# Optimization experiments

Hardware: AMD Instinct MI355X
Metric: run time of the kernel (lower is better)

Reference implementation:

```python
import jax, jax.numpy as jnp
import numpy as np

IN_F, OUT_F = 256, 256
GRID, ORDER = 5, 3
K = GRID + ORDER + 1  # 9 knots
EPS_MINMAX = 1e-7     # K.epsilon()
EPS_BN = 1e-3         # keras BatchNormalization default epsilon


def setup_inputs() -> dict:
    key = jax.random.key(0)
    ks = jax.random.split(key, 4)
    x = jax.random.normal(ks[0], (32, 32, 32, IN_F), dtype=jnp.float32)
    he = lambda k, shape, fan_in: jax.random.normal(k, shape, jnp.float32) * np.sqrt(2.0 / fan_in)
    base_weight = he(ks[1], (IN_F, OUT_F), IN_F)
    spline_weight = he(ks[2], (OUT_F, IN_F, K), IN_F * K)
    spline_scaler = jnp.ones((OUT_F, IN_F), jnp.float32)
    return {
        'x': x,
        'base_weight': base_weight,
        'spline_weight': spline_weight,
        'spline_scaler': spline_scaler,
        'bn_base_gamma': jnp.ones((OUT_F,), jnp.float32),
        'bn_base_beta': jnp.zeros((OUT_F,), jnp.float32),
        'bn_base_mean': jnp.zeros((OUT_F,), jnp.float32),
        'bn_base_var': jnp.ones((OUT_F,), jnp.float32),
        'bn_spline_gamma': jnp.ones((OUT_F,), jnp.float32),
        'bn_spline_beta': jnp.zeros((OUT_F,), jnp.float32),
        'bn_spline_mean': jnp.zeros((OUT_F,), jnp.float32),
        'bn_spline_var': jnp.ones((OUT_F,), jnp.float32),
    }


def _bn(z, gamma, beta, mean, var):
    # Keras BatchNormalization, inference mode (training=False)
    return gamma * (z - mean) * jax.lax.rsqrt(var + EPS_BN) + beta


def reference(x, base_weight, spline_weight, spline_scaler,
              bn_base_gamma, bn_base_beta, bn_base_mean, bn_base_var,
              bn_spline_gamma, bn_spline_beta, bn_spline_mean, bn_spline_var):
    B, H, W, _ = x.shape
    xf = x.reshape(-1, IN_F)  # [N, in]

    # base path: GEMM -> BN -> SiLU
    base = xf @ base_weight
    base = jax.nn.silu(_bn(base, bn_base_gamma, bn_base_beta, bn_base_mean, bn_base_var))

    # min-max normalize per feature over the flattened batch
    x_min = jnp.min(xf, axis=0, keepdims=True)
    x_max = jnp.max(xf, axis=0, keepdims=True)
    xn = (xf - x_min) / (x_max - x_min + EPS_MINMAX)

    # triangle basis: relu(1 - |x - knot|), knots = linspace(-1, 1, K)
    knots = jnp.linspace(-1.0, 1.0, K, dtype=jnp.float32)
    basis = jnp.maximum(0.0, 1.0 - jnp.abs(xn[:, :, None] - knots[None, None, :]))  # [N, in, K]

    # scaled spline weight, flattened GEMM
    w = (spline_weight * spline_scaler[:, :, None]).reshape(OUT_F, IN_F * K)  # [out, in*K]
    spline = basis.reshape(-1, IN_F * K) @ w.T  # [N, out]
    spline = _bn(spline, bn_spline_gamma, bn_spline_beta, bn_spline_mean, bn_spline_var)

    out = base + spline
    return out.reshape(B, H, W, OUT_F)
```

## Files before the change

### kernel.cpp

```cpp
#include <hip/hip_runtime.h>
#include <stdint.h>
#include <stddef.h>

typedef _Float16 h2 __attribute__((ext_vector_type(2)));
typedef _Float16 h8 __attribute__((ext_vector_type(8)));
typedef float f4 __attribute__((ext_vector_type(4)));

union Hfrag { h2 p[4]; h8 v; };

#define WS_PMIN   0
#define WS_PMAX   524288
#define WS_BT     0
#define WS_SMALL  1310720
#define WS_MINV   (WS_SMALL + 0)
#define WS_SCALEV (WS_SMALL + 1024)
#define WS_BSC    (WS_SMALL + 2048)
#define WS_BSH    (WS_SMALL + 3072)
#define WS_SSC    (WS_SMALL + 4096)
#define WS_SSH    (WS_SMALL + 5120)

__global__ __launch_bounds__(256) void kan_minmax(const float* __restrict__ x,
                                                  float* __restrict__ pmin,
                                                  float* __restrict__ pmax) {
  __shared__ f4 smn[4][64], smx[4][64];
  const int b = blockIdx.x, t = threadIdx.x;
  const int fq = t & 63, rg = t >> 6;
  const float* p = x + (size_t)b * 64 * 256 + (size_t)rg * 16 * 256 + fq * 4;
  f4 mn = (f4)(3.402823466e38f), mx = (f4)(-3.402823466e38f);
#pragma unroll
  for (int j = 0; j < 16; ++j) {
    f4 v = *(const f4*)(p + (size_t)j * 256);
    mn = __builtin_elementwise_min(mn, v);
    mx = __builtin_elementwise_max(mx, v);
  }
  smn[rg][fq] = mn; smx[rg][fq] = mx;
  __syncthreads();
  if (rg == 0) {
#pragma unroll
    for (int g = 1; g < 4; ++g) {
      mn = __builtin_elementwise_min(mn, smn[g][fq]);
      mx = __builtin_elementwise_max(mx, smx[g][fq]);
    }
    *(f4*)(pmin + (size_t)b * 256 + fq * 4) = mn;
    *(f4*)(pmax + (size_t)b * 256 + fq * 4) = mx;
  }
}

__global__ __launch_bounds__(256) void kan_finalize(
    const float* __restrict__ pmin, const float* __restrict__ pmax,
    const float* __restrict__ g1, const float* __restrict__ b1,
    const float* __restrict__ m1, const float* __restrict__ v1,
    const float* __restrict__ g2, const float* __restrict__ b2,
    const float* __restrict__ m2, const float* __restrict__ v2,
    float* __restrict__ minv, float* __restrict__ scalev,
    float* __restrict__ bscv, float* __restrict__ bshv,
    float* __restrict__ sscv, float* __restrict__ sshv) {
  __shared__ float smn[4][64], smx[4][64];
  const int t = threadIdx.x;
  const int ol = t & 63, pg = t >> 6;
  const int o = blockIdx.x * 64 + ol;
  float mn = 3.402823466e38f, mx = -3.402823466e38f;
  for (int p = pg * 128; p < pg * 128 + 128; ++p) {
    mn = fminf(mn, pmin[(size_t)p * 256 + o]);
    mx = fmaxf(mx, pmax[(size_t)p * 256 + o]);
  }
  smn[pg][ol] = mn; smx[pg][ol] = mx;
  __syncthreads();
  if (pg == 0) {
#pragma unroll
    for (int g = 1; g < 4; ++g) {
      mn = fminf(mn, smn[g][ol]);
      mx = fmaxf(mx, smx[g][ol]);
    }
    minv[o] = mn;
    scalev[o] = 1.0f / (mx - mn + 1e-7f);
    const float bs = g1[o] / sqrtf(v1[o] + 1e-3f);
    bscv[o] = bs;
    bshv[o] = b1[o] - m1[o] * bs;
    const float ss = g2[o] / sqrtf(v2[o] + 1e-3f);
    sscv[o] = ss;
    sshv[o] = b2[o] - m2[o] * ss;
  }
}

__global__ __launch_bounds__(256) void kan_buildw(
    const float* __restrict__ spline_w, const float* __restrict__ spline_s,
    const float* __restrict__ base_w, _Float16* __restrict__ Bt) {
  const int gid = blockIdx.x * 256 + threadIdx.x;
  const int f = gid * 4;
  const int ks = f >> 13;
  const int rem = f & 8191;
  const int half = rem >> 12;
  const int rem2 = rem & 4095;
  const int o = rem2 >> 5;
  const int kk = rem2 & 31;
  const int og = half * 128 + o;
  float v[4];
  if (ks < 72) {
    const int k = ks >> 3;
    const int i0 = ((ks & 7) << 5) + kk;
#pragma unroll
    for (int j = 0; j < 4; ++j) {
      const int i = i0 + j;
      v[j] = spline_w[(size_t)(og * 256 + i) * 9 + k] * spline_s[og * 256 + i];
    }
  } else {
    const int i0 = (ks - 72) * 32 + kk;
#pragma unroll
    for (int j = 0; j < 4; ++j) {
      const int i = i0 + j;
      v[j] = base_w[(size_t)i * 256 + og];
    }
  }
  union { _Float16 h[4]; uint2 u; } pk;
#pragma unroll
  for (int j = 0; j < 4; ++j) pk.h[j] = (_Float16)v[j];
  *(uint2*)(Bt + f) = pk.u;
}

__global__ __launch_bounds__(256, 2) void kan_gemm(
    const float* __restrict__ x, const _Float16* __restrict__ Bt,
    const float* __restrict__ minv, const float* __restrict__ scalev,
    const float* __restrict__ bscv, const float* __restrict__ bshv,
    const float* __restrict__ sscv, const float* __restrict__ sshv,
    float* __restrict__ out) {
  const int tid = threadIdx.x;
  const int lane = tid & 63;
  const int wv = tid >> 6;
  const int wm = wv >> 1, wn = wv & 1;
  const int lr = lane & 15, lg = lane >> 4;
  const int mt = blockIdx.x & 255, nt = blockIdx.x >> 8;

  const int rowA = mt * 128 + wm * 64 + lr;
  const int colB = wn * 64 + lr;

  f4 accS[4][4], accB[4][4];
#pragma unroll
  for (int m = 0; m < 4; ++m)
#pragma unroll
    for (int n = 0; n < 4; ++n) { accS[m][n] = (f4)0.0f; accB[m][n] = (f4)0.0f; }

  const char* btbase = (const char*)Bt + (size_t)nt * 8192 + (size_t)colB * 64 + (size_t)lg * 16;

  f4 xa[4], xb[4], mn0, mn1, sc0, sc1;

  {
    const int ib = lg * 8;
#pragma unroll
    for (int m = 0; m < 4; ++m) {
      const float* px = x + (size_t)(rowA + m * 16) * 256 + ib;
      xa[m] = *(const f4*)px; xb[m] = *(const f4*)(px + 4);
    }
    mn0 = *(const f4*)(minv + ib);  mn1 = *(const f4*)(minv + ib + 4);
    sc0 = *(const f4*)(scalev + ib); sc1 = *(const f4*)(scalev + ib + 4);
  }

#pragma unroll 1
  for (int ic = 0; ic < 8; ++ic) {
    Hfrag xn[4];
#pragma unroll
    for (int m = 0; m < 4; ++m) {
      f4 na = (xa[m] - mn0) * sc0;
      f4 nb = (xb[m] - mn1) * sc1;
      xn[m].p[0][0] = (_Float16)na.x; xn[m].p[0][1] = (_Float16)na.y;
      xn[m].p[1][0] = (_Float16)na.z; xn[m].p[1][1] = (_Float16)na.w;
      xn[m].p[2][0] = (_Float16)nb.x; xn[m].p[2][1] = (_Float16)nb.y;
      xn[m].p[3][0] = (_Float16)nb.z; xn[m].p[3][1] = (_Float16)nb.w;
    }
#pragma unroll
    for (int it = 0; it < 9; ++it) {
      const int cks = (it < 8) ? ((it + 1) * 8 + ic) : (72 + ic);
      const char* bp = btbase + (size_t)cks * 16384;
      Hfrag bf[4];
#pragma unroll
      for (int n = 0; n < 4; ++n)
        bf[n].v = *(const h8*)(bp + n * 1024);
      if (it < 8) {
        const float t = -1.0f + 0.25f * (float)(it + 1);
        const _Float16 c1 = (_Float16)(1.0f + t);
        const _Float16 c2 = (_Float16)(1.0f - t);
        h2 hc1; hc1[0] = c1; hc1[1] = c1;
        h2 hc2; hc2[0] = c2; hc2[1] = c2;
        h2 hz;  hz[0] = (_Float16)0.0f; hz[1] = (_Float16)0.0f;
        Hfrag af[4];
#pragma unroll
        for (int m = 0; m < 4; ++m) {
#pragma unroll
          for (int q = 0; q < 4; ++q) {
            h2 xv = xn[m].p[q];
            h2 u = hc1 - xv;
            h2 w = hc2 + xv;
            af[m].p[q] = __builtin_elementwise_max(__builtin_elementwise_min(u, w), hz);
          }
        }
#pragma unroll
        for (int m = 0; m < 4; ++m)
#pragma unroll
          for (int n = 0; n < 4; ++n)
            accS[m][n] = __builtin_amdgcn_mfma_f32_16x16x32_f16(af[m].v, bf[n].v, accS[m][n], 0, 0, 0);
      } else {
        Hfrag af[4];
#pragma unroll
        for (int m = 0; m < 4; ++m) {
          af[m].p[0][0] = (_Float16)xa[m].x; af[m].p[0][1] = (_Float16)xa[m].y;
          af[m].p[1][0] = (_Float16)xa[m].z; af[m].p[1][1] = (_Float16)xa[m].w;
          af[m].p[2][0] = (_Float16)xb[m].x; af[m].p[2][1] = (_Float16)xb[m].y;
          af[m].p[3][0] = (_Float16)xb[m].z; af[m].p[3][1] = (_Float16)xb[m].w;
        }
#pragma unroll
        for (int m = 0; m < 4; ++m)
#pragma unroll
          for (int n = 0; n < 4; ++n)
            accB[m][n] = __builtin_amdgcn_mfma_f32_16x16x32_f16(af[m].v, bf[n].v, accB[m][n], 0, 0, 0);
        if (ic < 7) {
          const int ib = (ic + 1) * 32 + lg * 8;
#pragma unroll
          for (int m = 0; m < 4; ++m) {
            const float* px = x + (size_t)(rowA + m * 16) * 256 + ib;
            xa[m] = *(const f4*)px; xb[m] = *(const f4*)(px + 4);
          }
          mn0 = *(const f4*)(minv + ib);  mn1 = *(const f4*)(minv + ib + 4);
          sc0 = *(const f4*)(scalev + ib); sc1 = *(const f4*)(scalev + ib + 4);
        }
      }
    }
  }

#pragma unroll
  for (int n = 0; n < 4; ++n) {
    const int col = nt * 128 + colB + n * 16;
    const float vbs = bscv[col], vbh = bshv[col];
    const float vss = sscv[col], vsh = sshv[col];
#pragma unroll
    for (int m = 0; m < 4; ++m) {
      const int row0 = mt * 128 + wm * 64 + m * 16 + lg * 4;
#pragma unroll
      for (int r = 0; r < 4; ++r) {
        const float zb = accB[m][n][r] * vbs + vbh;
        const float si = zb / (1.0f + __expf(-zb));
        const float val = si + accS[m][n][r] * vss + vsh;
        out[(size_t)(row0 + r) * 256 + col] = val;
      }
    }
  }
}

extern "C" void kernel_launch(void* const* d_in, const int* in_sizes, int n_in,
                              void* d_out, int out_size, void* d_ws, size_t ws_size,
                              hipStream_t stream) {
  const float* x        = (const float*)d_in[0];
  const float* base_w   = (const float*)d_in[1];
  const float* spline_w = (const float*)d_in[2];
  const float* spline_s = (const float*)d_in[3];
  const float* g1 = (const float*)d_in[4];
  const float* b1 = (const float*)d_in[5];
  const float* m1 = (const float*)d_in[6];
  const float* v1 = (const float*)d_in[7];
  const float* g2 = (const float*)d_in[8];
  const float* b2 = (const float*)d_in[9];
  const float* m2 = (const float*)d_in[10];
  const float* v2 = (const float*)d_in[11];
  float* out = (float*)d_out;
  char* ws = (char*)d_ws;

  float* pmin   = (float*)(ws + WS_PMIN);
  float* pmax   = (float*)(ws + WS_PMAX);
  _Float16* Bt  = (_Float16*)(ws + WS_BT);
  float* minv   = (float*)(ws + WS_MINV);
  float* scalev = (float*)(ws + WS_SCALEV);
  float* bscv   = (float*)(ws + WS_BSC);
  float* bshv   = (float*)(ws + WS_BSH);
  float* sscv   = (float*)(ws + WS_SSC);
  float* sshv   = (float*)(ws + WS_SSH);

  kan_minmax<<<512, 256, 0, stream>>>(x, pmin, pmax);
  kan_finalize<<<4, 256, 0, stream>>>(pmin, pmax, g1, b1, m1, v1, g2, b2, m2, v2,
                                      minv, scalev, bscv, bshv, sscv, sshv);
  kan_buildw<<<640, 256, 0, stream>>>(spline_w, spline_s, base_w, Bt);
  kan_gemm<<<512, 256, 0, stream>>>(x, Bt, minv, scalev, bscv, bshv, sscv, sshv, out);
}
```

Baseline: 167.2 us.

## Re-express triangle basis as ReLU hinge basis to shrink spline GEMM K

Since xn is in [0,1], only knots 1..8 matter, and the hat functions are rewritten as a constant, a linear term and three ReLU hinges relu(x - b_j) on raw x. The spline K dimension drops from 8 to 4 blocks per input, and the per-knot min/max/sub work becomes one sub plus a max. Weight build folds the combined coefficients, scale and constant term (C0) into a 4-slice Bt and the BN shift, and B-fragment loads are software-prefetched one step ahead. In exchange the hinge thresholds are computed in fp16 in absolute x units, which may change precision, and the build kernel now does a shared-memory reduction.

```diff
diff --git a/kernel.cpp b/kernel.cpp
--- a/kernel.cpp
+++ b/kernel.cpp
@@ -11,13 +11,14 @@
 #define WS_PMIN   0
 #define WS_PMAX   524288
 #define WS_BT     0
-#define WS_SMALL  1310720
-#define WS_MINV   (WS_SMALL + 0)
-#define WS_SCALEV (WS_SMALL + 1024)
-#define WS_BSC    (WS_SMALL + 2048)
-#define WS_BSH    (WS_SMALL + 3072)
-#define WS_SSC    (WS_SMALL + 4096)
-#define WS_SSH    (WS_SMALL + 5120)
+#define WS_SMALL  1048576
+#define WS_SCALEV (WS_SMALL + 0)
+#define WS_BKN    (WS_SMALL + 1024)
+#define WS_C0     (WS_SMALL + 3072)
+#define WS_BSC    (WS_SMALL + 4096)
+#define WS_BSH    (WS_SMALL + 5120)
+#define WS_SSC    (WS_SMALL + 6144)
+#define WS_SSH    (WS_SMALL + 7168)
 
 __global__ __launch_bounds__(256) void kan_minmax(const float* __restrict__ x,
                                                   float* __restrict__ pmin,
@@ -52,7 +53,7 @@
     const float* __restrict__ m1, const float* __restrict__ v1,
     const float* __restrict__ g2, const float* __restrict__ b2,
     const float* __restrict__ m2, const float* __restrict__ v2,
-    float* __restrict__ minv, float* __restrict__ scalev,
+    float* __restrict__ scalev, _Float16* __restrict__ bkn,
     float* __restrict__ bscv, float* __restrict__ bshv,
     float* __restrict__ sscv, float* __restrict__ sshv) {
   __shared__ float smn[4][64], smx[4][64];
@@ -72,8 +73,12 @@
       mn = fminf(mn, smn[g][ol]);
       mx = fmaxf(mx, smx[g][ol]);
     }
-    minv[o] = mn;
-    scalev[o] = 1.0f / (mx - mn + 1e-7f);
+    const float rng = mx - mn + 1e-7f;
+    scalev[o] = 1.0f / rng;
+    const float step = 0.25f * rng;
+#pragma unroll
+    for (int j = 0; j < 4; ++j)
+      bkn[j * 256 + o] = (_Float16)(mn + step * (float)j);
     const float bs = g1[o] / sqrtf(v1[o] + 1e-3f);
     bscv[o] = bs;
     bshv[o] = b1[o] - m1[o] * bs;
@@ -85,42 +90,43 @@
 
 __global__ __launch_bounds__(256) void kan_buildw(
     const float* __restrict__ spline_w, const float* __restrict__ spline_s,
-    const float* __restrict__ base_w, _Float16* __restrict__ Bt) {
-  const int gid = blockIdx.x * 256 + threadIdx.x;
-  const int f = gid * 4;
-  const int ks = f >> 13;
-  const int rem = f & 8191;
-  const int half = rem >> 12;
-  const int rem2 = rem & 4095;
-  const int o = rem2 >> 5;
-  const int kk = rem2 & 31;
-  const int og = half * 128 + o;
-  float v[4];
-  if (ks < 72) {
-    const int k = ks >> 3;
-    const int i0 = ((ks & 7) << 5) + kk;
-#pragma unroll
-    for (int j = 0; j < 4; ++j) {
-      const int i = i0 + j;
-      v[j] = spline_w[(size_t)(og * 256 + i) * 9 + k] * spline_s[og * 256 + i];
-    }
-  } else {
-    const int i0 = (ks - 72) * 32 + kk;
-#pragma unroll
-    for (int j = 0; j < 4; ++j) {
-      const int i = i0 + j;
-      v[j] = base_w[(size_t)i * 256 + og];
-    }
-  }
-  union { _Float16 h[4]; uint2 u; } pk;
-#pragma unroll
-  for (int j = 0; j < 4; ++j) pk.h[j] = (_Float16)v[j];
-  *(uint2*)(Bt + f) = pk.u;
+    const float* __restrict__ base_w, const float* __restrict__ scalev,
+    _Float16* __restrict__ Bt, float* __restrict__ C0) {
+  const int og = blockIdx.x;
+  const int i  = threadIdx.x;
+  const float* wp = spline_w + (size_t)(og * 256 + i) * 9;
+  const float w1 = wp[1], w2 = wp[2], w3 = wp[3], w4 = wp[4];
+  const float w5 = wp[5], w6 = wp[6], w7 = wp[7], w8 = wp[8];
+  const float s  = spline_s[og * 256 + i];
+  const float sc = scalev[i];
+  const float wp0 = 0.25f*w1 + 0.5f*w2 + 0.75f*w3 + w4 + 0.75f*w5 + 0.5f*w6 + 0.25f*w7;
+  float wj[4];
+  wj[0] = (w5 + w6 + w7 + w8) - (w1 + w2 + w3 + w4);
+  wj[1] = w1 - 2.0f * w5;
+  wj[2] = w2 - 2.0f * w6;
+  wj[3] = w3 - 2.0f * w7;
+  const float ssc = s * sc;
+  const int half = og >> 7, o = og & 127, ic = i >> 5, kk = i & 31;
+#pragma unroll
+  for (int j = 0; j < 4; ++j) {
+    const int ks = j * 8 + ic;
+    Bt[((size_t)(ks * 2 + half) * 128 + o) * 32 + kk] = (_Float16)(wj[j] * ssc);
+  }
+  Bt[((size_t)((32 + ic) * 2 + half) * 128 + o) * 32 + kk] =
+      (_Float16)base_w[(size_t)i * 256 + og];
+  __shared__ float red[256];
+  red[i] = wp0 * s;
+  __syncthreads();
+  for (int st = 128; st > 0; st >>= 1) {
+    if (i < st) red[i] += red[i + st];
+    __syncthreads();
+  }
+  if (i == 0) C0[og] = red[0];
 }
 
 __global__ __launch_bounds__(256, 2) void kan_gemm(
     const float* __restrict__ x, const _Float16* __restrict__ Bt,
-    const float* __restrict__ minv, const float* __restrict__ scalev,
+    const _Float16* __restrict__ bkn, const float* __restrict__ C0,
     const float* __restrict__ bscv, const float* __restrict__ bshv,
     const float* __restrict__ sscv, const float* __restrict__ sshv,
     float* __restrict__ out) {
@@ -142,8 +148,9 @@
 
   const char* btbase = (const char*)Bt + (size_t)nt * 8192 + (size_t)colB * 64 + (size_t)lg * 16;
 
-  f4 xa[4], xb[4], mn0, mn1, sc0, sc1;
-
+  h2 hz; hz[0] = (_Float16)0.0f; hz[1] = (_Float16)0.0f;
+
+  f4 xa[4], xb[4];
   {
     const int ib = lg * 8;
 #pragma unroll
@@ -151,77 +158,70 @@
       const float* px = x + (size_t)(rowA + m * 16) * 256 + ib;
       xa[m] = *(const f4*)px; xb[m] = *(const f4*)(px + 4);
     }
-    mn0 = *(const f4*)(minv + ib);  mn1 = *(const f4*)(minv + ib + 4);
-    sc0 = *(const f4*)(scalev + ib); sc1 = *(const f4*)(scalev + ib + 4);
   }
 
 #pragma unroll 1
   for (int ic = 0; ic < 8; ++ic) {
-    Hfrag xn[4];
+    Hfrag bb[4];
+#pragma unroll
+    for (int j = 0; j < 4; ++j)
+      bb[j].v = *(const h8*)(bkn + j * 256 + ic * 32 + lg * 8);
+
+    Hfrag xh[4];
 #pragma unroll
     for (int m = 0; m < 4; ++m) {
-      f4 na = (xa[m] - mn0) * sc0;
-      f4 nb = (xb[m] - mn1) * sc1;
-      xn[m].p[0][0] = (_Float16)na.x; xn[m].p[0][1] = (_Float16)na.y;
-      xn[m].p[1][0] = (_Float16)na.z; xn[m].p[1][1] = (_Float16)na.w;
-      xn[m].p[2][0] = (_Float16)nb.x; xn[m].p[2][1] = (_Float16)nb.y;
-      xn[m].p[3][0] = (_Float16)nb.z; xn[m].p[3][1] = (_Float16)nb.w;
-    }
-#pragma unroll
-    for (int it = 0; it < 9; ++it) {
-      const int cks = (it < 8) ? ((it + 1) * 8 + ic) : (72 + ic);
-      const char* bp = btbase + (size_t)cks * 16384;
-      Hfrag bf[4];
-#pragma unroll
-      for (int n = 0; n < 4; ++n)
-        bf[n].v = *(const h8*)(bp + n * 1024);
-      if (it < 8) {
-        const float t = -1.0f + 0.25f * (float)(it + 1);
-        const _Float16 c1 = (_Float16)(1.0f + t);
-        const _Float16 c2 = (_Float16)(1.0f - t);
-        h2 hc1; hc1[0] = c1; hc1[1] = c1;
-        h2 hc2; hc2[0] = c2; hc2[1] = c2;
-        h2 hz;  hz[0] = (_Float16)0.0f; hz[1] = (_Float16)0.0f;
+      xh[m].p[0][0] = (_Float16)xa[m].x; xh[m].p[0][1] = (_Float16)xa[m].y;
+      xh[m].p[1][0] = (_Float16)xa[m].z; xh[m].p[1][1] = (_Float16)xa[m].w;
+      xh[m].p[2][0] = (_Float16)xb[m].x; xh[m].p[2][1] = (_Float16)xb[m].y;
+      xh[m].p[3][0] = (_Float16)xb[m].z; xh[m].p[3][1] = (_Float16)xb[m].w;
+    }
+
+    if (ic < 7) {
+      const int ib = (ic + 1) * 32 + lg * 8;
+#pragma unroll
+      for (int m = 0; m < 4; ++m) {
+        const float* px = x + (size_t)(rowA + m * 16) * 256 + ib;
+        xa[m] = *(const f4*)px; xb[m] = *(const f4*)(px + 4);
+      }
+    }
+
+    const char* bpic = btbase + (size_t)ic * 16384;
+    Hfrag bf[4];
+#pragma unroll
+    for (int n = 0; n < 4; ++n) bf[n].v = *(const h8*)(bpic + n * 1024);
+
+#pragma unroll
+    for (int it = 0; it < 5; ++it) {
+      Hfrag bnx[4];
+      if (it < 4) {
+        const char* bp = bpic + (size_t)(it + 1) * 131072;
+#pragma unroll
+        for (int n = 0; n < 4; ++n) bnx[n].v = *(const h8*)(bp + n * 1024);
+      }
+      if (it < 4) {
         Hfrag af[4];
 #pragma unroll
-        for (int m = 0; m < 4; ++m) {
+        for (int m = 0; m < 4; ++m)
 #pragma unroll
           for (int q = 0; q < 4; ++q) {
-            h2 xv = xn[m].p[q];
-            h2 u = hc1 - xv;
-            h2 w = hc2 + xv;
-            af[m].p[q] = __builtin_elementwise_max(__builtin_elementwise_min(u, w), hz);
+            h2 d = xh[m].p[q] - bb[it].p[q];
+            af[m].p[q] = __builtin_elementwise_max(d, hz);
           }
-        }
 #pragma unroll
         for (int m = 0; m < 4; ++m)
 #pragma unroll
           for (int n = 0; n < 4; ++n)
             accS[m][n] = __builtin_amdgcn_mfma_f32_16x16x32_f16(af[m].v, bf[n].v, accS[m][n], 0, 0, 0);
       } else {
-        Hfrag af[4];
-#pragma unroll
-        for (int m = 0; m < 4; ++m) {
-          af[m].p[0][0] = (_Float16)xa[m].x; af[m].p[0][1] = (_Float16)xa[m].y;
-          af[m].p[1][0] = (_Float16)xa[m].z; af[m].p[1][1] = (_Float16)xa[m].w;
-          af[m].p[2][0] = (_Float16)xb[m].x; af[m].p[2][1] = (_Float16)xb[m].y;
-          af[m].p[3][0] = (_Float16)xb[m].z; af[m].p[3][1] = (_Float16)xb[m].w;
-        }
 #pragma unroll
         for (int m = 0; m < 4; ++m)
 #pragma unroll
           for (int n = 0; n < 4; ++n)
-            accB[m][n] = __builtin_amdgcn_mfma_f32_16x16x32_f16(af[m].v, bf[n].v, accB[m][n], 0, 0, 0);
-        if (ic < 7) {
-          const int ib = (ic + 1) * 32 + lg * 8;
-#pragma unroll
-          for (int m = 0; m < 4; ++m) {
-            const float* px = x + (size_t)(rowA + m * 16) * 256 + ib;
-            xa[m] = *(const f4*)px; xb[m] = *(const f4*)(px + 4);
-          }
-          mn0 = *(const f4*)(minv + ib);  mn1 = *(const f4*)(minv + ib + 4);
-          sc0 = *(const f4*)(scalev + ib); sc1 = *(const f4*)(scalev + ib + 4);
-        }
+            accB[m][n] = __builtin_amdgcn_mfma_f32_16x16x32_f16(xh[m].v, bf[n].v, accB[m][n], 0, 0, 0);
+      }
+      if (it < 4) {
+#pragma unroll
+        for (int n = 0; n < 4; ++n) bf[n] = bnx[n];
       }
     }
   }
@@ -230,7 +230,8 @@
   for (int n = 0; n < 4; ++n) {
     const int col = nt * 128 + colB + n * 16;
     const float vbs = bscv[col], vbh = bshv[col];
-    const float vss = sscv[col], vsh = sshv[col];
+    const float vss = sscv[col];
+    const float vsh = sshv[col] + vss * C0[col];
 #pragma unroll
     for (int m = 0; m < 4; ++m) {
       const int row0 = mt * 128 + wm * 64 + m * 16 + lg * 4;
@@ -263,19 +264,20 @@
   float* out = (float*)d_out;
   char* ws = (char*)d_ws;
 
-  float* pmin   = (float*)(ws + WS_PMIN);
-  float* pmax   = (float*)(ws + WS_PMAX);
-  _Float16* Bt  = (_Float16*)(ws + WS_BT);
-  float* minv   = (float*)(ws + WS_MINV);
-  float* scalev = (float*)(ws + WS_SCALEV);
-  float* bscv   = (float*)(ws + WS_BSC);
-  float* bshv   = (float*)(ws + WS_BSH);
-  float* sscv   = (float*)(ws + WS_SSC);
-  float* sshv   = (float*)(ws + WS_SSH);
+  float* pmin     = (float*)(ws + WS_PMIN);
+  float* pmax     = (float*)(ws + WS_PMAX);
+  _Float16* Bt    = (_Float16*)(ws + WS_BT);
+  float* scalev   = (float*)(ws + WS_SCALEV);
+  _Float16* bkn   = (_Float16*)(ws + WS_BKN);
+  float* C0       = (float*)(ws + WS_C0);
+  float* bscv     = (float*)(ws + WS_BSC);
+  float* bshv     = (float*)(ws + WS_BSH);
+  float* sscv     = (float*)(ws + WS_SSC);
+  float* sshv     = (float*)(ws + WS_SSH);
 
   kan_minmax<<<512, 256, 0, stream>>>(x, pmin, pmax);
   kan_finalize<<<4, 256, 0, stream>>>(pmin, pmax, g1, b1, m1, v1, g2, b2, m2, v2,
-                                      minv, scalev, bscv, bshv, sscv, sshv);
-  kan_buildw<<<640, 256, 0, stream>>>(spline_w, spline_s, base_w, Bt);
-  kan_gemm<<<512, 256, 0, stream>>>(x, Bt, minv, scalev, bscv, bshv, sscv, sshv, out);
-}
+                                      scalev, bkn, bscv, bshv, sscv, sshv);
+  kan_buildw<<<256, 256, 0, stream>>>(spline_w, spline_s, base_w, scalev, Bt, C0);
+  kan_gemm<<<512, 256, 0, stream>>>(x, Bt, bkn, C0, bscv, bshv, sscv, sshv, out);
+}
```

Result: slower. 183.8 us (+9.9%).
